# Kernel tuning notes

Measured on AMD Instinct MI355X. Metric: run time of the kernel, lower is better.

The kernel has to match this reference:

```python
import jax, jax.numpy as jnp
import numpy as np

NUM_ITEMS = 50000
EMBED_DIM = 100
HIDDEN_DIM = 200
BATCH = 1024
SEQ_LEN = 200


def setup_inputs() -> dict:
    key = jax.random.key(0)
    ks = jax.random.split(key, 8)
    q = jax.random.randint(ks[0], (BATCH, SEQ_LEN), 0, NUM_ITEMS, dtype=jnp.int32)
    embed = jax.random.normal(ks[1], (NUM_ITEMS, EMBED_DIM), jnp.float32) * 0.05
    # GRU weights, concatenated along gate axis in order (r, z, n)
    Wi = jax.random.normal(ks[2], (EMBED_DIM, 3 * HIDDEN_DIM), jnp.float32) * (1.0 / np.sqrt(EMBED_DIM))
    bi = jnp.zeros((3 * HIDDEN_DIM,), jnp.float32)  # input-side biases (flax dense_i has bias)
    Wh = jax.random.normal(ks[3], (HIDDEN_DIM, 3 * HIDDEN_DIM), jnp.float32) * (1.0 / np.sqrt(HIDDEN_DIM))
    bhn = jnp.zeros((HIDDEN_DIM,), jnp.float32)  # only the 'hn' hidden dense has a bias in flax GRUCell
    Wo = jax.random.normal(ks[4], (HIDDEN_DIM, NUM_ITEMS), jnp.float32) * (1.0 / np.sqrt(HIDDEN_DIM))
    bo = jnp.zeros((NUM_ITEMS,), jnp.float32)
    return {"q": q, "embed": embed, "Wi": Wi, "bi": bi, "Wh": Wh, "bhn": bhn, "Wo": Wo, "bo": bo}


def reference(q, embed, Wi, bi, Wh, bhn, Wo, bo):
    # mask padding id 0, then embed
    not_zero = (q != 0).astype(jnp.float32)[..., None]        # [B,T,1]
    x = jnp.take(embed, q, axis=0) * not_zero                 # [B,T,E]
    H = Wh.shape[0]

    def step(h, xt):
        gi = xt @ Wi + bi                                     # [B,3H]
        gh = h @ Wh                                           # [B,3H]
        ir, iz, inn = jnp.split(gi, 3, axis=-1)
        hr, hz, hn = jnp.split(gh, 3, axis=-1)
        r = jax.nn.sigmoid(ir + hr)
        z = jax.nn.sigmoid(iz + hz)
        n = jnp.tanh(inn + r * (hn + bhn))
        h_new = (1.0 - z) * n + z * h                          # flax GRUCell update
        return h_new, None

    h0 = jnp.zeros((q.shape[0], H), jnp.float32)
    xT = jnp.swapaxes(x, 0, 1)                                # [T,B,E]
    h_last, _ = jax.lax.scan(step, h0, xT)
    return h_last @ Wo + bo                                    # [B, num_items]
```

## Files before the change

### kernel.cpp

```cpp
#include <hip/hip_runtime.h>

#define BATCH 1024
#define TT    200
#define EE    100
#define HH    200
#define GG    600
#define NI    50000
#define NKT   7
#define KPAD  224
#define HSTR  264
#define NTILE3 3125
#define NTW   50
#define KTW   4

typedef _Float16 half8 __attribute__((ext_vector_type(8)));
typedef _Float16 half4v __attribute__((ext_vector_type(4)));
typedef float   float4v __attribute__((ext_vector_type(4)));

static __device__ __forceinline__ float4v mfma16(half8 a, half8 b, float4v c) {
    return __builtin_amdgcn_mfma_f32_16x16x32_f16(a, b, c, 0, 0, 0);
}

#if __has_builtin(__builtin_amdgcn_rcpf)
static __device__ __forceinline__ float fastrcp(float x) { return __builtin_amdgcn_rcpf(x); }
#else
static __device__ __forceinline__ float fastrcp(float x) { return 1.f / x; }
#endif

static __device__ __forceinline__ float sigm(float x) {
    return fastrcp(1.f + __expf(-x));
}
static __device__ __forceinline__ float tanh_fast(float x) {
    float e = __expf(2.f * fabsf(x));
    float t = 1.f - 2.f * fastrcp(e + 1.f);
    return __builtin_copysignf(t, x);
}

__global__ __launch_bounds__(64) void repack_wi(const float* __restrict__ Wi,
                                                const float* __restrict__ bi,
                                                half8* __restrict__ Wif,
                                                float* __restrict__ biP) {
    const int bx   = blockIdx.x;
    const int kt   = bx & 3;
    const int nt   = bx >> 2;
    const int lane = threadIdx.x;
    const int l15  = lane & 15;
    const int lhi  = lane >> 4;
    const int np   = nt * 16 + l15;
    const int c    = np >> 2;
    const int g    = np & 3;
    half8 v;
    #pragma unroll
    for (int j = 0; j < 8; ++j) {
        int k = kt * 32 + lhi * 8 + j;
        float w = (k < EE && g < 3) ? Wi[(size_t)k * GG + g * HH + c] : 0.f;
        v[j] = (_Float16)w;
    }
    Wif[(size_t)bx * 64 + lane] = v;
    if (kt == 0 && lhi == 0)
        biP[np] = (g < 3) ? bi[g * HH + c] : 0.f;
}

__global__ __launch_bounds__(256) void ewi_mfma(const float* __restrict__ embed,
                                                const half8* __restrict__ Wif,
                                                const float* __restrict__ biP,
                                                _Float16* __restrict__ EWi16) {
    const int tid  = threadIdx.x;
    const int w    = tid >> 6;
    const int lane = tid & 63;
    const int l15  = lane & 15;
    const int lhi  = lane >> 4;

    const int mt = blockIdx.x * 4 + w;
    if (mt >= NTILE3) return;
    const int i0 = mt * 16;

    half8 a[KTW];
    #pragma unroll
    for (int kt = 0; kt < KTW; ++kt) {
        const int k0 = kt * 32 + lhi * 8;
        const float* er = embed + (size_t)(i0 + l15) * EE + k0;
        #pragma unroll
        for (int j = 0; j < 8; ++j)
            a[kt][j] = (k0 + j < EE) ? (_Float16)er[j] : (_Float16)0.f;
    }

    #pragma unroll 2
    for (int nt = 0; nt < NTW; ++nt) {
        const half8* bf = Wif + (size_t)nt * KTW * 64 + lane;
        float4v acc = (float4v){0.f, 0.f, 0.f, 0.f};
        #pragma unroll
        for (int kt = 0; kt < KTW; ++kt)
            acc = mfma16(a[kt], bf[kt * 64], acc);
        const float biv = biP[nt * 16 + l15];
        #pragma unroll
        for (int r = 0; r < 4; ++r) {
            const int row = i0 + lhi * 4 + r;
            float val = acc[r] + biv;
            if (row == 0) val = biv;
            EWi16[(size_t)row * 800 + nt * 16 + l15] = (_Float16)val;
        }
    }
}

__global__ __launch_bounds__(64) void repack_whf(const float* __restrict__ Wh,
                                                 half8* __restrict__ Whf) {
    const int bx   = blockIdx.x;
    const int kt   = bx % NKT;
    const int tile = bx / NKT;
    const int g    = tile / 16;
    const int tc   = tile % 16;
    const int lane = threadIdx.x;
    const int col  = tc * 16 + (lane & 15);
    half8 v;
    #pragma unroll
    for (int j = 0; j < 8; ++j) {
        int k = kt * 32 + (lane >> 4) * 8 + j;
        float w = (k < HH && col < HH) ? Wh[(size_t)k * GG + g * HH + col] : 0.f;
        v[j] = (_Float16)w;
    }
    Whf[(size_t)bx * 64 + lane] = v;
}

__global__ __launch_bounds__(512, 2) void scan_mfma(const int* __restrict__ q,
                                                    const _Float16* __restrict__ EWi16,
                                                    const half8* __restrict__ Whf,
                                                    const float* __restrict__ bhn,
                                                    _Float16* __restrict__ h16g) {
    __shared__ __align__(16) _Float16 hbuf[2][16 * HSTR];
    __shared__ __align__(16) float accbuf[48 * 16 * 4];
    __shared__ int qs[4][TT];

    const int tid  = threadIdx.x;
    const int w    = tid >> 6;
    const int lane = tid & 63;
    const int l15  = lane & 15;
    const int lhi  = lane >> 4;
    const int b0   = blockIdx.x * 4;

    for (int idx = tid; idx < 2 * 16 * HSTR; idx += 512)
        ((_Float16*)hbuf)[idx] = (_Float16)0.f;
    for (int idx = tid; idx < 4 * TT; idx += 512) {
        int b = idx / TT, t = idx % TT;
        qs[b][t] = q[(size_t)(b0 + b) * TT + t];
    }

    half8 wb[3][2][7];
    #pragma unroll
    for (int g = 0; g < 3; ++g) {
        #pragma unroll
        for (int c2 = 0; c2 < 2; ++c2) {
            const int tc = w + c2 * 8;
            #pragma unroll
            for (int kt = 0; kt < NKT; ++kt)
                wb[g][c2][kt] = Whf[((size_t)(g * 16 + tc) * NKT + kt) * 64 + lane];
        }
    }

    const int col0 = w * 16 + l15;
    const int col1 = 128 + w * 16 + l15;
    const bool v1  = (col1 < HH);
    const int colw1 = v1 ? col1 : 236;
    const float bh0 = bhn[col0];
    const float bh1 = v1 ? bhn[col1] : 0.f;

    float hreg0 = 0.f, hreg1 = 0.f;

    __syncthreads();

    half4v giA0, giA1, giB0, giB1;
    #define LOADGI(d0, d1, tt) do {                                          \
        const int qv = qs[lhi][tt];                                          \
        const _Float16* ew = EWi16 + (size_t)qv * 800;                       \
        d0 = *(const half4v*)(ew + col0 * 4);                                \
        d1 = *(const half4v*)(ew + col1 * 4);                                \
    } while (0)

    LOADGI(giA0, giA1, 0);
    LOADGI(giB0, giB1, 1);

    #define STEP(CUR, NXT, G0, G1, TLOAD) do {                               \
        float4v acc[3][2];                                                   \
        _Pragma("unroll")                                                    \
        for (int g = 0; g < 3; ++g)                                          \
            _Pragma("unroll")                                                \
            for (int c2 = 0; c2 < 2; ++c2)                                   \
                acc[g][c2] = (float4v){0.f, 0.f, 0.f, 0.f};                  \
        const _Float16* hb = &hbuf[CUR][0];                                  \
        _Pragma("unroll")                                                    \
        for (int kt = 0; kt < NKT; ++kt) {                                   \
            const half8 af = *(const half8*)(hb + l15 * HSTR + kt * 32 + lhi * 8); \
            _Pragma("unroll")                                                \
            for (int g = 0; g < 3; ++g) {                                    \
                acc[g][0] = mfma16(af, wb[g][0][kt], acc[g][0]);             \
                acc[g][1] = mfma16(af, wb[g][1][kt], acc[g][1]);             \
            }                                                                \
        }                                                                    \
                \
        if (lane < 16) {                                                     \
            _Pragma("unroll")                                                \
            for (int g = 0; g < 3; ++g)                                      \
                _Pragma("unroll")                                            \
                for (int c2 = 0; c2 < 2; ++c2)                               \
                    *(float4v*)&accbuf[(((g * 16) + w + c2 * 8) * 16 + l15) * 4] = acc[g][c2]; \
        }                                                                    \
                              \
        _Float16* hn = &hbuf[NXT][0];                                        \
        {                                                                    \
            const int base0 = ((w) * 16 + l15) * 4 + lhi;                    \
            const int base1 = ((w + 8) * 16 + l15) * 4 + lhi;                \
            float aR0 = accbuf[0 * 1024 + base0];                            \
            float aZ0 = accbuf[1 * 1024 + base0];                            \
            float aN0 = accbuf[2 * 1024 + base0];                            \
            float aR1 = accbuf[0 * 1024 + base1];                            \
            float aZ1 = accbuf[1 * 1024 + base1];                            \
            float aN1 = accbuf[2 * 1024 + base1];                            \
            float r0 = sigm((float)G0[0] + aR0);                             \
            float z0 = sigm((float)G0[1] + aZ0);                             \
            float n0 = tanh_fast((float)G0[2] + r0 * (aN0 + bh0));           \
            float hv0 = (1.f - z0) * n0 + z0 * hreg0;                        \
            hreg0 = hv0;                                                     \
            hn[lhi * HSTR + col0] = (_Float16)hv0;                           \
            float r1 = sigm((float)G1[0] + aR1);                             \
            float z1 = sigm((float)G1[1] + aZ1);                             \
            float n1 = tanh_fast((float)G1[2] + r1 * (aN1 + bh1));           \
            float hv1 = (1.f - z1) * n1 + z1 * hreg1;                        \
            hreg1 = hv1;                                                     \
            hn[lhi * HSTR + colw1] = (_Float16)hv1;                          \
        }                                                                    \
         \
        {                                                                    \
            const int tl = (TLOAD) < TT ? (TLOAD) : (TT - 1);                \
            LOADGI(G0, G1, tl);                                              \
        }                                                                    \
        __syncthreads();                                                     \
    } while (0)

    for (int t = 0; t < TT; t += 2) {
        STEP(0, 1, giA0, giA1, t + 2);
        STEP(1, 0, giB0, giB1, t + 3);
    }
    #undef STEP
    #undef LOADGI

    for (int idx = tid; idx < 4 * KPAD; idx += 512) {
        int b = idx / KPAD, k = idx % KPAD;
        h16g[(size_t)(b0 + b) * KPAD + k] = hbuf[0][b * HSTR + k];
    }
}

__global__ __launch_bounds__(256) void out_mfma(const _Float16* __restrict__ h16g,
                                                const float* __restrict__ Wo,
                                                const float* __restrict__ bo,
                                                float* __restrict__ out) {
    const int tid  = threadIdx.x;
    const int w    = tid >> 6;
    const int lane = tid & 63;
    const int l15  = lane & 15;
    const int lhi  = lane >> 4;

    const int nt   = blockIdx.x * 4 + w;
    const bool live = (nt < NTILE3);
    const int ntc  = live ? nt : (NTILE3 - 1);
    const int col  = ntc * 16 + l15;

    half8 wb[7];
    #pragma unroll
    for (int kt = 0; kt < NKT; ++kt) {
        #pragma unroll
        for (int j = 0; j < 8; ++j) {
            int k = kt * 32 + lhi * 8 + j;
            wb[kt][j] = (k < HH) ? (_Float16)Wo[(size_t)k * NI + col] : (_Float16)0.f;
        }
    }
    const float bov = bo[col];

    for (int mt = 0; mt < BATCH / 16; ++mt) {
        const _Float16* hrow = h16g + (size_t)(mt * 16 + l15) * KPAD + lhi * 8;
        float4v acc = (float4v){0.f, 0.f, 0.f, 0.f};
        #pragma unroll
        for (int kt = 0; kt < NKT; ++kt) {
            const half8 af = *(const half8*)(hrow + kt * 32);
            acc = mfma16(af, wb[kt], acc);
        }
        if (live) {
            #pragma unroll
            for (int r = 0; r < 4; ++r) {
                int row = mt * 16 + lhi * 4 + r;
                out[(size_t)row * NI + col] = acc[r] + bov;
            }
        }
    }
}

extern "C" void kernel_launch(void* const* d_in, const int* in_sizes, int n_in,
                              void* d_out, int out_size, void* d_ws, size_t ws_size,
                              hipStream_t stream) {
    const int*   q     = (const int*)d_in[0];
    const float* embed = (const float*)d_in[1];
    const float* Wi    = (const float*)d_in[2];
    const float* bi    = (const float*)d_in[3];
    const float* Wh    = (const float*)d_in[4];
    const float* bhn   = (const float*)d_in[5];
    const float* Wo    = (const float*)d_in[6];
    const float* bo    = (const float*)d_in[7];
    float* out = (float*)d_out;

    _Float16* EWi16 = (_Float16*)d_out;
    half8*    Whf   = (half8*)((char*)d_out + 120000000);
    half8*    Wif   = (half8*)((char*)d_out + 121000000);
    float*    biP   = (float*)((char*)d_out + 122000000);
    _Float16* h16g  = (_Float16*)d_ws;

    repack_wi<<<NTW * KTW, 64, 0, stream>>>(Wi, bi, Wif, biP);
    repack_whf<<<48 * NKT, 64, 0, stream>>>(Wh, Whf);
    ewi_mfma<<<(NTILE3 + 3) / 4, 256, 0, stream>>>(embed, Wif, biP, EWi16);
    scan_mfma<<<BATCH / 4, 512, 0, stream>>>(q, EWi16, Whf, bhn, h16g);
    out_mfma<<<(NTILE3 + 3) / 4, 256, 0, stream>>>(h16g, Wo, bo, out);
}
```

Baseline: 430.1 us.

## Fuse repack kernels, double tiles per wave in GEMMs, pad accbuf layout

Merges the two weight-repack kernels into a single launch, cutting one kernel launch. The embedding-projection and output GEMM kernels now have each wave compute two 16-wide tiles, so each loaded B fragment (or A fragment) feeds two MFMAs and half as many waves are launched. The scan kernel's shared accumulator buffer is transposed to a row-major layout with a stride of 49 to reduce LDS bank conflicts. The extra tiles raise register pressure per wave and lower occupancy in the GEMM kernels.

```diff
diff --git a/kernel.cpp b/kernel.cpp
--- a/kernel.cpp
+++ b/kernel.cpp
@@ -36,29 +36,48 @@
     return __builtin_copysignf(t, x);
 }
 
-__global__ __launch_bounds__(64) void repack_wi(const float* __restrict__ Wi,
-                                                const float* __restrict__ bi,
-                                                half8* __restrict__ Wif,
-                                                float* __restrict__ biP) {
+__global__ __launch_bounds__(64) void repack_all(const float* __restrict__ Wi,
+                                                 const float* __restrict__ bi,
+                                                 const float* __restrict__ Wh,
+                                                 half8* __restrict__ Wif,
+                                                 float* __restrict__ biP,
+                                                 half8* __restrict__ Whf) {
     const int bx   = blockIdx.x;
-    const int kt   = bx & 3;
-    const int nt   = bx >> 2;
     const int lane = threadIdx.x;
     const int l15  = lane & 15;
     const int lhi  = lane >> 4;
-    const int np   = nt * 16 + l15;
-    const int c    = np >> 2;
-    const int g    = np & 3;
-    half8 v;
-    #pragma unroll
-    for (int j = 0; j < 8; ++j) {
-        int k = kt * 32 + lhi * 8 + j;
-        float w = (k < EE && g < 3) ? Wi[(size_t)k * GG + g * HH + c] : 0.f;
-        v[j] = (_Float16)w;
-    }
-    Wif[(size_t)bx * 64 + lane] = v;
-    if (kt == 0 && lhi == 0)
-        biP[np] = (g < 3) ? bi[g * HH + c] : 0.f;
+    if (bx < NTW * KTW) {
+        const int kt = bx & 3;
+        const int nt = bx >> 2;
+        const int np = nt * 16 + l15;
+        const int c  = np >> 2;
+        const int g  = np & 3;
+        half8 v;
+        #pragma unroll
+        for (int j = 0; j < 8; ++j) {
+            int k = kt * 32 + lhi * 8 + j;
+            float w = (k < EE && g < 3) ? Wi[(size_t)k * GG + g * HH + c] : 0.f;
+            v[j] = (_Float16)w;
+        }
+        Wif[(size_t)bx * 64 + lane] = v;
+        if (kt == 0 && lhi == 0)
+            biP[np] = (g < 3) ? bi[g * HH + c] : 0.f;
+    } else {
+        const int b2   = bx - NTW * KTW;
+        const int kt   = b2 % NKT;
+        const int tile = b2 / NKT;
+        const int g    = tile / 16;
+        const int tc   = tile % 16;
+        const int col  = tc * 16 + l15;
+        half8 v;
+        #pragma unroll
+        for (int j = 0; j < 8; ++j) {
+            int k = kt * 32 + lhi * 8 + j;
+            float w = (k < HH && col < HH) ? Wh[(size_t)k * GG + g * HH + col] : 0.f;
+            v[j] = (_Float16)w;
+        }
+        Whf[(size_t)b2 * 64 + lane] = v;
+    }
 }
 
 __global__ __launch_bounds__(256) void ewi_mfma(const float* __restrict__ embed,
@@ -71,55 +90,52 @@
     const int l15  = lane & 15;
     const int lhi  = lane >> 4;
 
-    const int mt = blockIdx.x * 4 + w;
-    if (mt >= NTILE3) return;
-    const int i0 = mt * 16;
-
-    half8 a[KTW];
+    const int mtb   = (blockIdx.x * 4 + w) * 2;
+    const bool liveA = (mtb < NTILE3);
+    const bool liveB = (mtb + 1 < NTILE3);
+    if (!liveA) return;
+    const int i0a = mtb * 16;
+    const int i0b = liveB ? (mtb + 1) * 16 : i0a;
+
+    half8 aA[KTW], aB[KTW];
     #pragma unroll
     for (int kt = 0; kt < KTW; ++kt) {
         const int k0 = kt * 32 + lhi * 8;
-        const float* er = embed + (size_t)(i0 + l15) * EE + k0;
-        #pragma unroll
-        for (int j = 0; j < 8; ++j)
-            a[kt][j] = (k0 + j < EE) ? (_Float16)er[j] : (_Float16)0.f;
-    }
-
-    #pragma unroll 2
+        const float* erA = embed + (size_t)(i0a + l15) * EE + k0;
+        const float* erB = embed + (size_t)(i0b + l15) * EE + k0;
+        #pragma unroll
+        for (int j = 0; j < 8; ++j) {
+            aA[kt][j] = (k0 + j < EE) ? (_Float16)erA[j] : (_Float16)0.f;
+            aB[kt][j] = (k0 + j < EE) ? (_Float16)erB[j] : (_Float16)0.f;
+        }
+    }
+
     for (int nt = 0; nt < NTW; ++nt) {
-        const half8* bf = Wif + (size_t)nt * KTW * 64 + lane;
-        float4v acc = (float4v){0.f, 0.f, 0.f, 0.f};
-        #pragma unroll
-        for (int kt = 0; kt < KTW; ++kt)
-            acc = mfma16(a[kt], bf[kt * 64], acc);
+        const half8* bfp = Wif + (size_t)nt * KTW * 64 + lane;
+        float4v accA = (float4v){0.f, 0.f, 0.f, 0.f};
+        float4v accB = (float4v){0.f, 0.f, 0.f, 0.f};
+        #pragma unroll
+        for (int kt = 0; kt < KTW; ++kt) {
+            const half8 bf = bfp[kt * 64];
+            accA = mfma16(aA[kt], bf, accA);
+            accB = mfma16(aB[kt], bf, accB);
+        }
         const float biv = biP[nt * 16 + l15];
         #pragma unroll
         for (int r = 0; r < 4; ++r) {
-            const int row = i0 + lhi * 4 + r;
-            float val = acc[r] + biv;
-            if (row == 0) val = biv;
-            EWi16[(size_t)row * 800 + nt * 16 + l15] = (_Float16)val;
-        }
-    }
-}
-
-__global__ __launch_bounds__(64) void repack_whf(const float* __restrict__ Wh,
-                                                 half8* __restrict__ Whf) {
-    const int bx   = blockIdx.x;
-    const int kt   = bx % NKT;
-    const int tile = bx / NKT;
-    const int g    = tile / 16;
-    const int tc   = tile % 16;
-    const int lane = threadIdx.x;
-    const int col  = tc * 16 + (lane & 15);
-    half8 v;
-    #pragma unroll
-    for (int j = 0; j < 8; ++j) {
-        int k = kt * 32 + (lane >> 4) * 8 + j;
-        float w = (k < HH && col < HH) ? Wh[(size_t)k * GG + g * HH + col] : 0.f;
-        v[j] = (_Float16)w;
-    }
-    Whf[(size_t)bx * 64 + lane] = v;
+            const int rowA = i0a + lhi * 4 + r;
+            float valA = accA[r] + biv;
+            if (rowA == 0) valA = biv;
+            EWi16[(size_t)rowA * 800 + nt * 16 + l15] = (_Float16)valA;
+        }
+        if (liveB) {
+            #pragma unroll
+            for (int r = 0; r < 4; ++r) {
+                const int rowB = i0b + lhi * 4 + r;
+                EWi16[(size_t)rowB * 800 + nt * 16 + l15] = (_Float16)(accB[r] + biv);
+            }
+        }
+    }
 }
 
 __global__ __launch_bounds__(512, 2) void scan_mfma(const int* __restrict__ q,
@@ -128,7 +144,7 @@
                                                     const float* __restrict__ bhn,
                                                     _Float16* __restrict__ h16g) {
     __shared__ __align__(16) _Float16 hbuf[2][16 * HSTR];
-    __shared__ __align__(16) float accbuf[48 * 16 * 4];
+    __shared__ __align__(16) float accbuf[16 * 49 * 4];
     __shared__ int qs[4][TT];
 
     const int tid  = threadIdx.x;
@@ -202,19 +218,18 @@
             for (int g = 0; g < 3; ++g)                                      \
                 _Pragma("unroll")                                            \
                 for (int c2 = 0; c2 < 2; ++c2)                               \
-                    *(float4v*)&accbuf[(((g * 16) + w + c2 * 8) * 16 + l15) * 4] = acc[g][c2]; \
+                    *(float4v*)&accbuf[((l15 * 49) + (g * 16 + w + c2 * 8)) * 4] = acc[g][c2]; \
         }                                                                    \
                               \
         _Float16* hn = &hbuf[NXT][0];                                        \
         {                                                                    \
-            const int base0 = ((w) * 16 + l15) * 4 + lhi;                    \
-            const int base1 = ((w + 8) * 16 + l15) * 4 + lhi;                \
-            float aR0 = accbuf[0 * 1024 + base0];                            \
-            float aZ0 = accbuf[1 * 1024 + base0];                            \
-            float aN0 = accbuf[2 * 1024 + base0];                            \
-            float aR1 = accbuf[0 * 1024 + base1];                            \
-            float aZ1 = accbuf[1 * 1024 + base1];                            \
-            float aN1 = accbuf[2 * 1024 + base1];                            \
+            const int rowb = l15 * 49 * 4 + lhi;                             \
+            float aR0 = accbuf[rowb + (0 * 16 + w) * 4];                     \
+            float aZ0 = accbuf[rowb + (1 * 16 + w) * 4];                     \
+            float aN0 = accbuf[rowb + (2 * 16 + w) * 4];                     \
+            float aR1 = accbuf[rowb + (0 * 16 + w + 8) * 4];                 \
+            float aZ1 = accbuf[rowb + (1 * 16 + w + 8) * 4];                 \
+            float aN1 = accbuf[rowb + (2 * 16 + w + 8) * 4];                 \
             float r0 = sigm((float)G0[0] + aR0);                             \
             float z0 = sigm((float)G0[1] + aZ0);                             \
             float n0 = tanh_fast((float)G0[2] + r0 * (aN0 + bh0));           \
@@ -259,35 +274,49 @@
     const int l15  = lane & 15;
     const int lhi  = lane >> 4;
 
-    const int nt   = blockIdx.x * 4 + w;
-    const bool live = (nt < NTILE3);
-    const int ntc  = live ? nt : (NTILE3 - 1);
-    const int col  = ntc * 16 + l15;
-
-    half8 wb[7];
+    const int ntb   = (blockIdx.x * 4 + w) * 2;
+    const bool liveA = (ntb < NTILE3);
+    const bool liveB = (ntb + 1 < NTILE3);
+    const int ntA = liveA ? ntb : (NTILE3 - 1);
+    const int ntB = liveB ? (ntb + 1) : (NTILE3 - 1);
+    const int colA = ntA * 16 + l15;
+    const int colB = ntB * 16 + l15;
+
+    half8 wbA[7], wbB[7];
     #pragma unroll
     for (int kt = 0; kt < NKT; ++kt) {
         #pragma unroll
         for (int j = 0; j < 8; ++j) {
             int k = kt * 32 + lhi * 8 + j;
-            wb[kt][j] = (k < HH) ? (_Float16)Wo[(size_t)k * NI + col] : (_Float16)0.f;
-        }
-    }
-    const float bov = bo[col];
+            wbA[kt][j] = (k < HH) ? (_Float16)Wo[(size_t)k * NI + colA] : (_Float16)0.f;
+            wbB[kt][j] = (k < HH) ? (_Float16)Wo[(size_t)k * NI + colB] : (_Float16)0.f;
+        }
+    }
+    const float bovA = bo[colA];
+    const float bovB = bo[colB];
 
     for (int mt = 0; mt < BATCH / 16; ++mt) {
         const _Float16* hrow = h16g + (size_t)(mt * 16 + l15) * KPAD + lhi * 8;
-        float4v acc = (float4v){0.f, 0.f, 0.f, 0.f};
+        float4v accA = (float4v){0.f, 0.f, 0.f, 0.f};
+        float4v accB = (float4v){0.f, 0.f, 0.f, 0.f};
         #pragma unroll
         for (int kt = 0; kt < NKT; ++kt) {
             const half8 af = *(const half8*)(hrow + kt * 32);
-            acc = mfma16(af, wb[kt], acc);
-        }
-        if (live) {
+            accA = mfma16(af, wbA[kt], accA);
+            accB = mfma16(af, wbB[kt], accB);
+        }
+        if (liveA) {
             #pragma unroll
             for (int r = 0; r < 4; ++r) {
                 int row = mt * 16 + lhi * 4 + r;
-                out[(size_t)row * NI + col] = acc[r] + bov;
+                out[(size_t)row * NI + colA] = accA[r] + bovA;
+            }
+        }
+        if (liveB) {
+            #pragma unroll
+            for (int r = 0; r < 4; ++r) {
+                int row = mt * 16 + lhi * 4 + r;
+                out[(size_t)row * NI + colB] = accB[r] + bovB;
             }
         }
     }
@@ -312,9 +341,8 @@
     float*    biP   = (float*)((char*)d_out + 122000000);
     _Float16* h16g  = (_Float16*)d_ws;
 
-    repack_wi<<<NTW * KTW, 64, 0, stream>>>(Wi, bi, Wif, biP);
-    repack_whf<<<48 * NKT, 64, 0, stream>>>(Wh, Whf);
-    ewi_mfma<<<(NTILE3 + 3) / 4, 256, 0, stream>>>(embed, Wif, biP, EWi16);
+    repack_all<<<NTW * KTW + 48 * NKT, 64, 0, stream>>>(Wi, bi, Wh, Wif, biP, Whf);
+    ewi_mfma<<<(NTILE3 / 2 + 3) / 4, 256, 0, stream>>>(embed, Wif, biP, EWi16);
     scan_mfma<<<BATCH / 4, 512, 0, stream>>>(q, EWi16, Whf, bhn, h16g);
-    out_mfma<<<(NTILE3 + 3) / 4, 256, 0, stream>>>(h16g, Wo, bo, out);
-}
+    out_mfma<<<(NTILE3 / 2 + 3) / 4 + 1, 256, 0, stream>>>(h16g, Wo, bo, out);
+}
```

After: 374.9 us. 12.8% less time.
